# Kernel optimization log

Measured on AMD Instinct MI355X. Metric: run time of the kernel, lower is better.

The kernel has to match this reference:

```python
import jax, jax.numpy as jnp
import numpy as np

QLEN, MLEN, BSZ = 1024, 1024, 8
D_MODEL, N_HEAD, D_HEAD = 512, 8, 64
KLEN = QLEN + MLEN
TAU = 1.0


def _rel_shift(x):
    # x: [qlen, klen, bsz, n_head] -- Transformer-XL relative shift
    q, k, b, n = x.shape
    zero_pad = jnp.zeros((q, 1, b, n), dtype=x.dtype)
    x_padded = jnp.concatenate([zero_pad, x], axis=1).reshape(k + 1, q, b, n)
    return x_padded[1:].reshape(q, k, b, n)


def setup_inputs() -> dict:
    key = jax.random.key(0)
    ks = jax.random.split(key, 8)
    w = jax.random.normal(ks[0], (QLEN, BSZ, D_MODEL), dtype=jnp.float32)
    r = jax.random.normal(ks[1], (KLEN, D_MODEL), dtype=jnp.float32)
    r_w_bias = jax.random.normal(ks[2], (N_HEAD, D_HEAD), dtype=jnp.float32) * 0.02
    r_r_bias = jax.random.normal(ks[3], (N_HEAD, D_HEAD), dtype=jnp.float32) * 0.02
    mems = jax.random.normal(ks[4], (MLEN, BSZ, D_MODEL), dtype=jnp.float32)
    W_qkv = jax.random.normal(ks[5], (D_MODEL, 3 * N_HEAD * D_HEAD), dtype=jnp.float32) * 0.02
    W_r = jax.random.normal(ks[6], (D_MODEL, N_HEAD * D_HEAD), dtype=jnp.float32) * 0.02
    W_o = jax.random.normal(ks[7], (N_HEAD * D_HEAD, D_MODEL), dtype=jnp.float32) * 0.02
    # causal mask with memory: query i can attend keys j <= i + MLEN
    i = jnp.arange(QLEN)[:, None]
    j = jnp.arange(KLEN)[None, :]
    attn_mask = (j > i + MLEN)[:, :, None]  # [qlen, klen, 1] bool, True = masked
    return {"w": w, "r": r, "r_w_bias": r_w_bias, "r_r_bias": r_r_bias,
            "mems": mems, "attn_mask": attn_mask,
            "W_qkv": W_qkv, "W_r": W_r, "W_o": W_o}


def reference(w, r, r_w_bias, r_r_bias, mems, attn_mask, W_qkv, W_r, W_o):
    qlen, bsz, d_model = w.shape
    n_head, d_head = r_w_bias.shape
    scale = 1.0 / np.sqrt(d_head).astype(np.float32)

    cat = jnp.concatenate([mems, w], axis=0)          # [klen, bsz, d_model]
    w_heads = cat @ W_qkv                              # [klen, bsz, 3*n*d]
    w_head_q, w_head_k, w_head_v = jnp.split(w_heads, 3, axis=-1)
    klen = w_head_k.shape[0]
    w_head_q = w_head_q[-qlen:].reshape(qlen, bsz, n_head, d_head)
    w_head_k = w_head_k.reshape(klen, bsz, n_head, d_head)
    w_head_v = w_head_v.reshape(klen, bsz, n_head, d_head)
    r_head_k = (r @ W_r).reshape(-1, n_head, d_head)   # [rlen, n, d]

    AC = jnp.einsum('ibnd,jbnd->ijbn', w_head_q + r_w_bias, w_head_k)
    BD = jnp.einsum('ibnd,jnd->ijbn', w_head_q + r_r_bias, r_head_k)
    BD = _rel_shift(BD)

    attn_score = (AC + BD) * scale                     # [q, k, b, n]
    mask4 = attn_mask[:, :, :, None]                   # [q, k, 1, 1]
    attn_score = jnp.where(mask4, -jnp.inf, attn_score)
    attn_prob = jax.nn.softmax(attn_score * TAU, axis=1)

    # attention entropy per head (no-grad in original)
    p_safe = jnp.where(mask4, 1.0, attn_prob)
    temp = -attn_prob * jnp.log(p_safe)
    attn_entropy = jax.lax.stop_gradient(jnp.mean(jnp.sum(temp, axis=1), axis=(0, 1)))  # [n_head]

    attn_vec = jnp.einsum('ijbn,jbnd->ibnd', attn_prob, w_head_v)
    attn_vec = attn_vec.reshape(qlen, bsz, n_head * d_head)
    attn_out = attn_vec @ W_o                          # [q, b, d_model]
    return attn_out, attn_entropy
```

## Files before the change

### kernel.cpp

```cpp
#include <hip/hip_runtime.h>
#include <hip/hip_bf16.h>


#define QLEN 1024
#define MLEN 1024
#define KLEN 2048
#define BSZ 8
#define DMODEL 512
#define NHEAD 8
#define DHEAD 64
#define SCALE 0.125f
#define RPAD 2176
#define RTHR 8.0f

#define B_QW   0u
#define B_QR   8388608u
#define B_K    16777216u
#define B_VT   33554432u
#define B_R    50331648u
#define B_AVB  52559872u
#define B_ENT  60948480u
#define B_ABF  60952576u
#define B_WQT  77729792u
#define B_RBF  79302656u
#define B_WRT  81399808u
#define B_WOT  81924096u

typedef short bf16x8 __attribute__((ext_vector_type(8)));
typedef float f32x4  __attribute__((ext_vector_type(4)));

#define SWZ(row, byte) ((((row) << 7) + (((((byte) >> 4) ^ ((row) & 7)) << 4)) + ((byte) & 15)))

__device__ __forceinline__ unsigned short f2bf(float f) {
    union { float f; unsigned int u; } v; v.f = f;
    unsigned int r = v.u + 0x7FFFu + ((v.u >> 16) & 1u);
    return (unsigned short)(r >> 16);
}

__global__ __launch_bounds__(256) void cvt_cat(const float* __restrict__ mems,
                                               const float* __restrict__ w,
                                               unsigned short* __restrict__ Abf) {
    size_t e = ((size_t)blockIdx.x * 256 + threadIdx.x) * 8;
    int m = (int)(e >> 9), k = (int)(e & 511);
    int t = m >> 3, b = m & 7;
    const float* src = (t < MLEN) ? mems + ((size_t)t * 8 + b) * 512 + k
                                  : w    + ((size_t)(t - MLEN) * 8 + b) * 512 + k;
    float4 v0 = *reinterpret_cast<const float4*>(src);
    float4 v1 = *reinterpret_cast<const float4*>(src + 4);
    ushort4 o0, o1;
    o0.x = f2bf(v0.x); o0.y = f2bf(v0.y); o0.z = f2bf(v0.z); o0.w = f2bf(v0.w);
    o1.x = f2bf(v1.x); o1.y = f2bf(v1.y); o1.z = f2bf(v1.z); o1.w = f2bf(v1.w);
    *reinterpret_cast<ushort4*>(Abf + e)     = o0;
    *reinterpret_cast<ushort4*>(Abf + e + 4) = o1;
}

__global__ __launch_bounds__(256) void cvt_r(const float* __restrict__ r,
                                             unsigned short* __restrict__ rbf) {
    size_t e = ((size_t)blockIdx.x * 256 + threadIdx.x) * 8;
    float4 v0 = *reinterpret_cast<const float4*>(r + e);
    float4 v1 = *reinterpret_cast<const float4*>(r + e + 4);
    ushort4 o0, o1;
    o0.x = f2bf(v0.x); o0.y = f2bf(v0.y); o0.z = f2bf(v0.z); o0.w = f2bf(v0.w);
    o1.x = f2bf(v1.x); o1.y = f2bf(v1.y); o1.z = f2bf(v1.z); o1.w = f2bf(v1.w);
    *reinterpret_cast<ushort4*>(rbf + e)     = o0;
    *reinterpret_cast<ushort4*>(rbf + e + 4) = o1;
}

__global__ __launch_bounds__(256) void tcvt(const float* __restrict__ S,
                                            unsigned short* __restrict__ D,
                                            int R, int C) {
    __shared__ float t[32][33];
    int bx = blockIdx.x * 32;
    int by = blockIdx.y * 32;
    int x = threadIdx.x & 31, y = threadIdx.x >> 5;
    #pragma unroll
    for (int q = 0; q < 4; ++q)
        t[y + q * 8][x] = S[(size_t)(by + y + q * 8) * C + bx + x];
    __syncthreads();
    #pragma unroll
    for (int q = 0; q < 4; ++q)
        D[(size_t)(bx + y + q * 8) * R + by + x] = f2bf(t[x][y + q * 8]);
}

__global__ void zpad_r(unsigned short* __restrict__ Rg) {
    int idx = blockIdx.x * 256 + threadIdx.x;
    int n = idx >> 10, o = idx & 1023;
    uint4 z = make_uint4(0, 0, 0, 0);
    *reinterpret_cast<uint4*>(Rg + ((size_t)n * RPAD + KLEN) * 64 + o * 8) = z;
}

template<int MODE>
__global__ __launch_bounds__(256) void gemm_mfma(const unsigned short* __restrict__ A,
                                                 const unsigned short* __restrict__ Bt,
                                                 const float* __restrict__ rwb,
                                                 const float* __restrict__ rrb,
                                                 unsigned short* __restrict__ QW,
                                                 unsigned short* __restrict__ QR,
                                                 unsigned short* __restrict__ Kg,
                                                 unsigned short* __restrict__ VT,
                                                 unsigned short* __restrict__ Rg,
                                                 float* __restrict__ Cout) {
    __shared__ unsigned short Als[128][72];
    __shared__ unsigned short Bls[128][72];
    const int tid = threadIdx.x;
    const int wv = tid >> 6, lane = tid & 63, lg = lane >> 4, lc = lane & 15;
    const int wr = wv >> 1, wc = wv & 1;
    const int n0 = blockIdx.x * 128;
    const int m0 = blockIdx.y * 128;

    f32x4 acc[4][4];
    #pragma unroll
    for (int mi = 0; mi < 4; ++mi)
        #pragma unroll
        for (int ni = 0; ni < 4; ++ni)
            acc[mi][ni] = (f32x4){0.f, 0.f, 0.f, 0.f};

    for (int k0 = 0; k0 < 512; k0 += 64) {
        __syncthreads();
        #pragma unroll
        for (int q = 0; q < 4; ++q) {
            int c = q * 256 + tid;
            int row = c >> 3, off = (c & 7) * 8;
            *reinterpret_cast<uint4*>(&Als[row][off]) =
                *reinterpret_cast<const uint4*>(A + (size_t)(m0 + row) * 512 + k0 + off);
            *reinterpret_cast<uint4*>(&Bls[row][off]) =
                *reinterpret_cast<const uint4*>(Bt + (size_t)(n0 + row) * 512 + k0 + off);
        }
        __syncthreads();
        #pragma unroll
        for (int kk = 0; kk < 2; ++kk) {
            bf16x8 af[4], bfr[4];
            #pragma unroll
            for (int mi = 0; mi < 4; ++mi)
                af[mi] = *reinterpret_cast<const bf16x8*>(&Als[64 * wr + 16 * mi + lc][32 * kk + lg * 8]);
            #pragma unroll
            for (int ni = 0; ni < 4; ++ni)
                bfr[ni] = *reinterpret_cast<const bf16x8*>(&Bls[64 * wc + 16 * ni + lc][32 * kk + lg * 8]);
            #pragma unroll
            for (int mi = 0; mi < 4; ++mi)
                #pragma unroll
                for (int ni = 0; ni < 4; ++ni)
                    acc[mi][ni] = __builtin_amdgcn_mfma_f32_16x16x32_bf16(af[mi], bfr[ni], acc[mi][ni], 0, 0, 0);
        }
    }

    #pragma unroll
    for (int mi = 0; mi < 4; ++mi) {
        #pragma unroll
        for (int ni = 0; ni < 4; ++ni) {
            const int n = n0 + 64 * wc + 16 * ni + lc;
            float bw = 0.f, br = 0.f;
            int region = 0, hn = 0, d = 0;
            if (MODE == 0) {
                region = n >> 9; int cr = n & 511; hn = cr >> 6; d = cr & 63;
                if (region == 0) { bw = rwb[hn * 64 + d]; br = rrb[hn * 64 + d]; }
            }
            #pragma unroll
            for (int reg = 0; reg < 4; ++reg) {
                const int m = m0 + 64 * wr + 16 * mi + lg * 4 + reg;
                const float val = acc[mi][ni][reg];
                if (MODE == 0) {
                    int t = m >> 3, b = m & 7, bn = b * 8 + hn;
                    if (region == 0) {
                        if (t >= MLEN) {
                            size_t base = ((size_t)bn * QLEN + (t - MLEN)) * 64 + d;
                            QW[base] = f2bf(val + bw);
                            QR[base] = f2bf(val + br);
                        }
                    } else if (region == 1) {
                        Kg[((size_t)bn * KLEN + t) * 64 + d] = f2bf(val);
                    } else {
                        VT[((size_t)bn * 64 + d) * KLEN + t] = f2bf(val);
                    }
                } else if (MODE == 1) {
                    Rg[((size_t)(n >> 6) * RPAD + m) * 64 + (n & 63)] = f2bf(val);
                } else {
                    Cout[(size_t)m * 512 + n] = val;
                }
            }
        }
    }
}

__global__ __launch_bounds__(512, 2) void attn_mfma(const unsigned short* __restrict__ QWg,
                                                    const unsigned short* __restrict__ QRg,
                                                    const unsigned short* __restrict__ Kg,
                                                    const unsigned short* __restrict__ VTg,
                                                    const unsigned short* __restrict__ Rg,
                                                    unsigned short* __restrict__ AVB,
                                                    float* __restrict__ ENT) {
    __shared__ __attribute__((aligned(16))) unsigned short Klds[64 * 64];
    __shared__ __attribute__((aligned(16))) unsigned short Rblds[192 * 64];
    __shared__ __attribute__((aligned(16))) unsigned short Vtlds[64 * 64];
    __shared__ __attribute__((aligned(16))) unsigned short Plds[128 * 64];

    const int tid = threadIdx.x;
    const int w = tid >> 6, lane = tid & 63, lg = lane >> 4, lc = lane & 15;
    const int n = blockIdx.x;
    const int b = blockIdx.y & 7;
    const int kq = blockIdx.y >> 3;
    const int iblk = (kq < 4) ? kq : 11 - kq;
    const int i0 = iblk * 128;
    const int bn = b * 8 + n;
    const int srow = tid >> 3;
    const int sch  = tid & 7;

    {
        const unsigned short* qwsrc = QWg + ((size_t)bn * QLEN + i0) * 64;
        const unsigned short* qrsrc = QRg + ((size_t)bn * QLEN + i0) * 64;
        #pragma unroll
        for (int q = 0; q < 2; ++q) {
            int row = srow + q * 64;
            *reinterpret_cast<uint4*>((char*)Rblds + SWZ(row, sch * 16)) =
                *reinterpret_cast<const uint4*>(qwsrc + (size_t)row * 64 + sch * 8);
            *reinterpret_cast<uint4*>((char*)Plds + SWZ(row, sch * 16)) =
                *reinterpret_cast<const uint4*>(qrsrc + (size_t)row * 64 + sch * 8);
        }
    }
    __syncthreads();
    bf16x8 aqw[2], aqr[2];
    #pragma unroll
    for (int k = 0; k < 2; ++k) {
        aqw[k] = *reinterpret_cast<const bf16x8*>((const char*)Rblds + SWZ(16 * w + lc, 64 * k + 16 * lg));
        aqr[k] = *reinterpret_cast<const bf16x8*>((const char*)Plds + SWZ(16 * w + lc, 64 * k + 16 * lg));
    }

    f32x4 Ofr[4];
    #pragma unroll
    for (int t = 0; t < 4; ++t) Ofr[t] = (f32x4){0.f, 0.f, 0.f, 0.f};
    float mreg[4] = {-1e30f, -1e30f, -1e30f, -1e30f};
    float lpart[4] = {0.f, 0.f, 0.f, 0.f};
    float tpart[4] = {0.f, 0.f, 0.f, 0.f};

    const int nj = 2 * iblk + 18;
    const unsigned short* kbase = Kg  + (size_t)bn * KLEN * 64;
    const unsigned short* vbase = VTg + (size_t)bn * 64 * KLEN;
    const unsigned short* rbase = Rg  + (size_t)n * RPAD * 64 + (size_t)(896 - i0) * 64;

    uint4 kr0, vr0, rr0, rr1, rr2;
    kr0 = *reinterpret_cast<const uint4*>(kbase + (size_t)srow * 64 + sch * 8);
    vr0 = *reinterpret_cast<const uint4*>(vbase + (size_t)srow * KLEN + sch * 8);
    rr0 = *reinterpret_cast<const uint4*>(rbase + (size_t)(srow)       * 64 + sch * 8);
    rr1 = *reinterpret_cast<const uint4*>(rbase + (size_t)(srow + 64)  * 64 + sch * 8);
    rr2 = *reinterpret_cast<const uint4*>(rbase + (size_t)(srow + 128) * 64 + sch * 8);

    for (int jt = 0; jt < nj; ++jt) {
        const int j0 = jt * 64;
        __syncthreads();

        *reinterpret_cast<uint4*>((char*)Klds  + SWZ(srow,       sch * 16)) = kr0;
        *reinterpret_cast<uint4*>((char*)Vtlds + SWZ(srow,       sch * 16)) = vr0;
        *reinterpret_cast<uint4*>((char*)Rblds + SWZ(srow,       sch * 16)) = rr0;
        *reinterpret_cast<uint4*>((char*)Rblds + SWZ(srow + 64,  sch * 16)) = rr1;
        *reinterpret_cast<uint4*>((char*)Rblds + SWZ(srow + 128, sch * 16)) = rr2;

        if (jt + 1 < nj) {
            const int j1 = j0 + 64;
            kr0 = *reinterpret_cast<const uint4*>(kbase + (size_t)(j1 + srow) * 64 + sch * 8);
            vr0 = *reinterpret_cast<const uint4*>(vbase + (size_t)srow * KLEN + j1 + sch * 8);
            rr0 = *reinterpret_cast<const uint4*>(rbase + (size_t)(j1 + srow)       * 64 + sch * 8);
            rr1 = *reinterpret_cast<const uint4*>(rbase + (size_t)(j1 + srow + 64)  * 64 + sch * 8);
            rr2 = *reinterpret_cast<const uint4*>(rbase + (size_t)(j1 + srow + 128) * 64 + sch * 8);
        }

        asm volatile("s_waitcnt lgkmcnt(0)" ::: "memory");
        __builtin_amdgcn_sched_barrier(0);
        __builtin_amdgcn_s_barrier();
        asm volatile("" ::: "memory");
        __builtin_amdgcn_sched_barrier(0);

        __builtin_amdgcn_s_setprio(1);
        f32x4 sfr[4];
        #pragma unroll
        for (int bj = 0; bj < 4; ++bj) {
            f32x4 acc = (f32x4){0.f, 0.f, 0.f, 0.f};
            #pragma unroll
            for (int k = 0; k < 2; ++k) {
                bf16x8 bk = *reinterpret_cast<const bf16x8*>((const char*)Klds + SWZ(16 * bj + lc, 64 * k + 16 * lg));
                acc = __builtin_amdgcn_mfma_f32_16x16x32_bf16(aqw[k], bk, acc, 0, 0, 0);
            }
            sfr[bj] = acc;
        }
        f32x4 g[5];
        const int sb = 112 - 16 * w;
        #pragma unroll
        for (int cb = 0; cb < 5; ++cb) {
            g[cb] = (f32x4){0.f, 0.f, 0.f, 0.f};
            #pragma unroll
            for (int k = 0; k < 2; ++k) {
                bf16x8 br = *reinterpret_cast<const bf16x8*>((const char*)Rblds + SWZ(sb + 16 * cb + lc, 64 * k + 16 * lg));
                g[cb] = __builtin_amdgcn_mfma_f32_16x16x32_bf16(aqr[k], br, g[cb], 0, 0, 0);
            }
        }
        __builtin_amdgcn_s_setprio(0);

        #pragma unroll
        for (int reg = 0; reg < 4; ++reg) {
            int r = lg * 4 + reg;
            int srcl = (lane & 48) | ((lc - r + 15) & 15);
            float gg[5];
            #pragma unroll
            for (int cb = 0; cb < 5; ++cb)
                gg[cb] = __shfl(g[cb][reg], srcl, 64);
            #pragma unroll
            for (int bj = 0; bj < 4; ++bj) {
                float gv = (lc <= r) ? gg[bj] : gg[bj + 1];
                sfr[bj][reg] = (sfr[bj][reg] + gv) * SCALE;
            }
        }
        if (jt >= nj - 2) {
            #pragma unroll
            for (int bj = 0; bj < 4; ++bj)
                #pragma unroll
                for (int reg = 0; reg < 4; ++reg) {
                    int ii = 16 * w + lg * 4 + reg;
                    int jj = 16 * bj + lc;
                    if (j0 + jj > i0 + ii + MLEN) sfr[bj][reg] = -1e30f;
                }
        }

        float pm[4];
        #pragma unroll
        for (int reg = 0; reg < 4; ++reg)
            pm[reg] = fmaxf(fmaxf(sfr[0][reg], sfr[1][reg]), fmaxf(sfr[2][reg], sfr[3][reg]));
        bool grow = (pm[0] > mreg[0] + RTHR) || (pm[1] > mreg[1] + RTHR) ||
                    (pm[2] > mreg[2] + RTHR) || (pm[3] > mreg[3] + RTHR);
        if (__any(grow)) {
            #pragma unroll
            for (int reg = 0; reg < 4; ++reg) {
                float gmax = pm[reg];
                gmax = fmaxf(gmax, __shfl_xor(gmax, 1));
                gmax = fmaxf(gmax, __shfl_xor(gmax, 2));
                gmax = fmaxf(gmax, __shfl_xor(gmax, 4));
                gmax = fmaxf(gmax, __shfl_xor(gmax, 8));
                float mo = mreg[reg], mn = fmaxf(mo, gmax);
                float fac = __expf(mo - mn);
                lpart[reg] *= fac; tpart[reg] *= fac; mreg[reg] = mn;
                Ofr[0][reg] *= fac; Ofr[1][reg] *= fac;
                Ofr[2][reg] *= fac; Ofr[3][reg] *= fac;
            }
        }
        #pragma unroll
        for (int reg = 0; reg < 4; ++reg) {
            float mn = mreg[reg];
            float le = 0.f, te = 0.f;
            int r = lg * 4 + reg;
            #pragma unroll
            for (int bj = 0; bj < 4; ++bj) {
                float e = __expf(sfr[bj][reg] - mn);
                le += e; te += e * sfr[bj][reg];
                *reinterpret_cast<unsigned short*>((char*)Plds + SWZ(16 * w + r, 2 * (16 * bj + lc))) = f2bf(e);
            }
            lpart[reg] += le;
            tpart[reg] += te;
        }
        asm volatile("s_waitcnt lgkmcnt(0)" ::: "memory");
        __builtin_amdgcn_sched_barrier(0);

        __builtin_amdgcn_s_setprio(1);
        #pragma unroll
        for (int k = 0; k < 2; ++k) {
            bf16x8 ap = *reinterpret_cast<const bf16x8*>((const char*)Plds + SWZ(16 * w + lc, 64 * k + 16 * lg));
            Ofr[0] = __builtin_amdgcn_mfma_f32_16x16x32_bf16(ap,
                *reinterpret_cast<const bf16x8*>((const char*)Vtlds + SWZ( 0 + lc, 64 * k + 16 * lg)), Ofr[0], 0, 0, 0);
            Ofr[1] = __builtin_amdgcn_mfma_f32_16x16x32_bf16(ap,
                *reinterpret_cast<const bf16x8*>((const char*)Vtlds + SWZ(16 + lc, 64 * k + 16 * lg)), Ofr[1], 0, 0, 0);
            Ofr[2] = __builtin_amdgcn_mfma_f32_16x16x32_bf16(ap,
                *reinterpret_cast<const bf16x8*>((const char*)Vtlds + SWZ(32 + lc, 64 * k + 16 * lg)), Ofr[2], 0, 0, 0);
            Ofr[3] = __builtin_amdgcn_mfma_f32_16x16x32_bf16(ap,
                *reinterpret_cast<const bf16x8*>((const char*)Vtlds + SWZ(48 + lc, 64 * k + 16 * lg)), Ofr[3], 0, 0, 0);
        }
        __builtin_amdgcn_s_setprio(0);
    }

    float lred[4], tred[4];
    #pragma unroll
    for (int reg = 0; reg < 4; ++reg) {
        float l = lpart[reg], t = tpart[reg];
        l += __shfl_xor(l, 1); l += __shfl_xor(l, 2); l += __shfl_xor(l, 4); l += __shfl_xor(l, 8);
        t += __shfl_xor(t, 1); t += __shfl_xor(t, 2); t += __shfl_xor(t, 4); t += __shfl_xor(t, 8);
        lred[reg] = l; tred[reg] = t;
    }

    #pragma unroll
    for (int reg = 0; reg < 4; ++reg) {
        int i = i0 + 16 * w + lg * 4 + reg;
        float inv = 1.f / lred[reg];
        unsigned short* dst = AVB + ((size_t)i * BSZ + b) * DMODEL + n * 64 + lc;
        dst[ 0] = f2bf(Ofr[0][reg] * inv);
        dst[16] = f2bf(Ofr[1][reg] * inv);
        dst[32] = f2bf(Ofr[2][reg] * inv);
        dst[48] = f2bf(Ofr[3][reg] * inv);
    }

    float h = 0.f;
    if (lc == 0) {
        #pragma unroll
        for (int reg = 0; reg < 4; ++reg)
            h += mreg[reg] + __logf(lred[reg]) - tred[reg] / lred[reg];
    }
    h += __shfl_xor(h, 1);  h += __shfl_xor(h, 2);  h += __shfl_xor(h, 4);
    h += __shfl_xor(h, 8);  h += __shfl_xor(h, 16); h += __shfl_xor(h, 32);
    __syncthreads();
    float* hred = reinterpret_cast<float*>(Klds);
    if (lane == 0) hred[w] = h;
    __syncthreads();
    if (tid == 0) {
        float s = 0.f;
        #pragma unroll
        for (int q = 0; q < 8; ++q) s += hred[q];
        ENT[bn * 8 + iblk] = s;
    }
}

__global__ void reduce_ent(const float* __restrict__ ent, float* __restrict__ out) {
    int n = threadIdx.x;
    if (n < NHEAD) {
        float s = 0.f;
        for (int b = 0; b < BSZ; ++b)
            for (int it = 0; it < 8; ++it)
                s += ent[(b * NHEAD + n) * 8 + it];
        out[(size_t)QLEN * BSZ * DMODEL + n] = s / (float)(QLEN * BSZ);
    }
}

extern "C" void kernel_launch(void* const* d_in, const int* in_sizes, int n_in,
                              void* d_out, int out_size, void* d_ws, size_t ws_size,
                              hipStream_t stream) {
    const float* w    = (const float*)d_in[0];
    const float* r    = (const float*)d_in[1];
    const float* rwb  = (const float*)d_in[2];
    const float* rrb  = (const float*)d_in[3];
    const float* mems = (const float*)d_in[4];
    const float* Wqkv = (const float*)d_in[6];
    const float* Wr   = (const float*)d_in[7];
    const float* Wo   = (const float*)d_in[8];
    float* out = (float*)d_out;
    char*  wsb = (char*)d_ws;

    unsigned short* QW  = (unsigned short*)(wsb + B_QW);
    unsigned short* QR  = (unsigned short*)(wsb + B_QR);
    unsigned short* Kg  = (unsigned short*)(wsb + B_K);
    unsigned short* VT  = (unsigned short*)(wsb + B_VT);
    unsigned short* Rg  = (unsigned short*)(wsb + B_R);
    unsigned short* AVB = (unsigned short*)(wsb + B_AVB);
    float* ENT = (float*)(wsb + B_ENT);
    unsigned short* ABF = (unsigned short*)(wsb + B_ABF);
    unsigned short* WQT = (unsigned short*)(wsb + B_WQT);
    unsigned short* RBF = (unsigned short*)(wsb + B_RBF);
    unsigned short* WRT = (unsigned short*)(wsb + B_WRT);
    unsigned short* WOT = (unsigned short*)(wsb + B_WOT);

    cvt_cat<<<4096, 256, 0, stream>>>(mems, w, ABF);
    cvt_r<<<512, 256, 0, stream>>>(r, RBF);
    tcvt<<<dim3(48, 16), 256, 0, stream>>>(Wqkv, WQT, 512, 1536);
    tcvt<<<dim3(16, 16), 256, 0, stream>>>(Wr, WRT, 512, 512);
    tcvt<<<dim3(16, 16), 256, 0, stream>>>(Wo, WOT, 512, 512);
    zpad_r<<<32, 256, 0, stream>>>(Rg);

    gemm_mfma<0><<<dim3(12, 128), 256, 0, stream>>>(ABF, WQT, rwb, rrb, QW, QR, Kg, VT, nullptr, nullptr);
    gemm_mfma<1><<<dim3(4, 16), 256, 0, stream>>>(RBF, WRT, nullptr, nullptr,
                                                  nullptr, nullptr, nullptr, nullptr, Rg, nullptr);

    attn_mfma<<<dim3(8, 64), 512, 0, stream>>>(QW, QR, Kg, VT, Rg, AVB, ENT);
    reduce_ent<<<1, 64, 0, stream>>>(ENT, out);

    gemm_mfma<2><<<dim3(4, 64), 256, 0, stream>>>(AVB, WOT, nullptr, nullptr,
                                                  nullptr, nullptr, nullptr, nullptr, nullptr, out);
}
```

Baseline: 239.3 us.

## Fold softmax scale and log2e into Q projection; remap GEMM blocks per XCD

```diff
diff --git a/kernel.cpp b/kernel.cpp
--- a/kernel.cpp
+++ b/kernel.cpp
@@ -9,9 +9,10 @@
 #define DMODEL 512
 #define NHEAD 8
 #define DHEAD 64
-#define SCALE 0.125f
 #define RPAD 2176
-#define RTHR 8.0f
+#define QSC  0.18033688011112042f
+#define RTHR 11.54f
+#define LN2F 0.6931471805599453f
 
 #define B_QW   0u
 #define B_QR   8388608u
@@ -105,8 +106,21 @@
     const int tid = threadIdx.x;
     const int wv = tid >> 6, lane = tid & 63, lg = lane >> 4, lc = lane & 15;
     const int wr = wv >> 1, wc = wv & 1;
-    const int n0 = blockIdx.x * 128;
-    const int m0 = blockIdx.y * 128;
+    int n0, m0;
+    if (MODE == 0) {
+        int id = blockIdx.x + 12 * blockIdx.y;
+        int xcd = id & 7, u = id >> 3;
+        n0 = (u % 12) * 128;
+        m0 = (32 * xcd + u / 12) * 128;
+    } else if (MODE == 2) {
+        int id = blockIdx.x + 4 * blockIdx.y;
+        int xcd = id & 7, u = id >> 3;
+        n0 = (u % 4) * 128;
+        m0 = (8 * xcd + u / 4) * 128;
+    } else {
+        n0 = blockIdx.x * 128;
+        m0 = blockIdx.y * 128;
+    }
 
     f32x4 acc[4][4];
     #pragma unroll
@@ -164,8 +178,8 @@
                     if (region == 0) {
                         if (t >= MLEN) {
                             size_t base = ((size_t)bn * QLEN + (t - MLEN)) * 64 + d;
-                            QW[base] = f2bf(val + bw);
-                            QR[base] = f2bf(val + br);
+                            QW[base] = f2bf((val + bw) * QSC);
+                            QR[base] = f2bf((val + br) * QSC);
                         }
                     } else if (region == 1) {
                         Kg[((size_t)bn * KLEN + t) * 64 + d] = f2bf(val);
@@ -305,7 +319,7 @@
             #pragma unroll
             for (int bj = 0; bj < 4; ++bj) {
                 float gv = (lc <= r) ? gg[bj] : gg[bj + 1];
-                sfr[bj][reg] = (sfr[bj][reg] + gv) * SCALE;
+                sfr[bj][reg] = sfr[bj][reg] + gv;
             }
         }
         if (jt >= nj - 2) {
@@ -334,7 +348,7 @@
                 gmax = fmaxf(gmax, __shfl_xor(gmax, 4));
                 gmax = fmaxf(gmax, __shfl_xor(gmax, 8));
                 float mo = mreg[reg], mn = fmaxf(mo, gmax);
-                float fac = __expf(mo - mn);
+                float fac = exp2f(mo - mn);
                 lpart[reg] *= fac; tpart[reg] *= fac; mreg[reg] = mn;
                 Ofr[0][reg] *= fac; Ofr[1][reg] *= fac;
                 Ofr[2][reg] *= fac; Ofr[3][reg] *= fac;
@@ -347,7 +361,7 @@
             int r = lg * 4 + reg;
             #pragma unroll
             for (int bj = 0; bj < 4; ++bj) {
-                float e = __expf(sfr[bj][reg] - mn);
+                float e = exp2f(sfr[bj][reg] - mn);
                 le += e; te += e * sfr[bj][reg];
                 *reinterpret_cast<unsigned short*>((char*)Plds + SWZ(16 * w + r, 2 * (16 * bj + lc))) = f2bf(e);
             }
@@ -397,7 +411,7 @@
     if (lc == 0) {
         #pragma unroll
         for (int reg = 0; reg < 4; ++reg)
-            h += mreg[reg] + __logf(lred[reg]) - tred[reg] / lred[reg];
+            h += mreg[reg] + log2f(lred[reg]) - tred[reg] / lred[reg];
     }
     h += __shfl_xor(h, 1);  h += __shfl_xor(h, 2);  h += __shfl_xor(h, 4);
     h += __shfl_xor(h, 8);  h += __shfl_xor(h, 16); h += __shfl_xor(h, 32);
@@ -409,7 +423,7 @@
         float s = 0.f;
         #pragma unroll
         for (int q = 0; q < 8; ++q) s += hred[q];
-        ENT[bn * 8 + iblk] = s;
+        ENT[bn * 8 + iblk] = s * LN2F;
     }
 }
 
```

Result: slower. 246.2 us (+2.9%).
